# Performance work log

Hardware: AMD Instinct MI355X
Metric: run time of the kernel (lower is better)

The kernel has to match this reference:

```python
import jax, jax.numpy as jnp
import numpy as np
import math

E = 2048         # n_embd
H = 16           # num query head pairs (num_heads)
HKV = 8          # num_kv_heads
NREP = H // HKV  # 2
HD = E // H // 2 # head_dim = 64
DEPTH = 12
LAMBDA_INIT = 0.8 - 0.6 * math.exp(-0.3 * DEPTH)
EPS = 1e-6


def setup_inputs() -> dict:
    key = jax.random.key(0)
    ks = jax.random.split(key, 10)
    s = lambda fan_in: 1.0 / np.sqrt(fan_in)
    return {
        "x": jax.random.normal(ks[0], (2, 2048, E), jnp.float32),
        "Wq": jax.random.normal(ks[1], (E, E), jnp.float32) * s(E),
        "Wk": jax.random.normal(ks[2], (E, E // NREP), jnp.float32) * s(E),
        "Wv": jax.random.normal(ks[3], (E, E // NREP), jnp.float32) * s(E),
        "Wo": jax.random.normal(ks[4], (E, E), jnp.float32) * s(E),
        "lam_q1": jax.random.normal(ks[5], (HD,), jnp.float32) * 0.1,
        "lam_k1": jax.random.normal(ks[6], (HD,), jnp.float32) * 0.1,
        "lam_q2": jax.random.normal(ks[7], (HD,), jnp.float32) * 0.1,
        "lam_k2": jax.random.normal(ks[8], (HD,), jnp.float32) * 0.1,
        "g": jnp.ones((2 * HD,), jnp.float32),  # RMSNorm weight
    }


def _rotary(x, cos, sin):
    # x: [B, T, nh, HD]; cos/sin: [T, HD//2]
    d = x.shape[-1] // 2
    x1, x2 = x[..., :d], x[..., d:]
    c = cos[None, :, None, :]
    si = sin[None, :, None, :]
    return jnp.concatenate([x1 * c + x2 * si, -x1 * si + x2 * c], axis=-1)


def reference(x, Wq, Wk, Wv, Wo, lam_q1, lam_k1, lam_q2, lam_k2, g):
    B, T, _ = x.shape
    q = (x @ Wq).reshape(B, T, 2 * H, HD)
    k = (x @ Wk).reshape(B, T, 2 * HKV, HD)
    v = (x @ Wv).reshape(B, T, HKV, 2 * HD)

    inv_freq = 1.0 / (10000.0 ** (jnp.arange(0, HD, 2, dtype=jnp.float32) / HD))
    freqs = jnp.arange(T, dtype=jnp.float32)[:, None] * inv_freq[None, :]
    cos, sin = jnp.cos(freqs), jnp.sin(freqs)
    q = _rotary(q, cos, sin)
    k = _rotary(k, cos, sin)

    q = jnp.transpose(q, (0, 2, 1, 3)) * (HD ** -0.5)   # [B, 2H, T, HD]
    k = jnp.repeat(jnp.transpose(k, (0, 2, 1, 3)), NREP, axis=1)  # [B, 2H, T, HD]
    v = jnp.repeat(jnp.transpose(v, (0, 2, 1, 3)), NREP, axis=1)  # [B, H, T, 2HD]

    scores = jnp.einsum('bhtd,bhsd->bhts', q, k)
    scores = jnp.nan_to_num(scores)
    mask = jnp.triu(jnp.full((T, T), -jnp.inf, scores.dtype), 1)
    scores = scores + mask
    p = jax.nn.softmax(scores.astype(jnp.float32), axis=-1).astype(scores.dtype)

    lam1 = jnp.exp(jnp.sum(lam_q1 * lam_k1))
    lam2 = jnp.exp(jnp.sum(lam_q2 * lam_k2))
    lam = lam1 - lam2 + LAMBDA_INIT

    p = p.reshape(B, H, 2, T, T)
    diff = p[:, :, 0] - lam * p[:, :, 1]               # [B, H, T, T]
    attn = jnp.einsum('bhts,bhsd->bhtd', diff, v)      # [B, H, T, 2HD]

    # RMSNorm over last dim (2*HD)
    attn = attn * jax.lax.rsqrt(jnp.mean(attn * attn, axis=-1, keepdims=True) + EPS) * g
    attn = attn * (1.0 - LAMBDA_INIT)
    attn = jnp.transpose(attn, (0, 2, 1, 3)).reshape(B, T, E)
    return attn @ Wo
```

## Files before the change

### kernel.cpp

```cpp
#include <hip/hip_runtime.h>

#define T_SEQ 2048

typedef __bf16 bf16x8 __attribute__((ext_vector_type(8)));
typedef float f32x4 __attribute__((ext_vector_type(4)));
typedef unsigned short u16;

__device__ __forceinline__ u16 f2b(float f) {
  unsigned u = __float_as_uint(f);
  unsigned r = 0x7fffu + ((u >> 16) & 1u);
  return (u16)((u + r) >> 16);
}
__device__ __forceinline__ float b2f(u16 v) {
  return __uint_as_float(((unsigned)v) << 16);
}
__device__ __forceinline__ f32x4 mfma16(bf16x8 a, bf16x8 b, f32x4 c) {
  return __builtin_amdgcn_mfma_f32_16x16x32_bf16(a, b, c, 0, 0, 0);
}
__device__ __forceinline__ unsigned pkhi(float lo, float hi) {
  return __builtin_amdgcn_perm(__float_as_uint(hi), __float_as_uint(lo), 0x07060302u);
}
#if defined(__has_builtin)
#if __has_builtin(__builtin_amdgcn_exp2f)
#define HAVE_RAW_EXP2 1
#endif
#endif
__device__ __forceinline__ float exp2r(float x) {
#ifdef HAVE_RAW_EXP2
  return __builtin_amdgcn_exp2f(x);
#else
  float r;
  asm("v_exp_f32 %0, %1" : "=v"(r) : "v"(x));
  return r;
#endif
}
__device__ __forceinline__ void glds16(const void* g, void* s) {
  __builtin_amdgcn_global_load_lds(
      (const __attribute__((address_space(1))) void*)(uintptr_t)g,
      (__attribute__((address_space(3))) void*)(unsigned)(uintptr_t)s, 16, 0, 0);
}

__global__ void lam_kernel(const float* __restrict__ q1, const float* __restrict__ k1,
                           const float* __restrict__ q2, const float* __restrict__ k2,
                           float* __restrict__ outp) {
  int l = threadIdx.x;
  float a = q1[l] * k1[l];
  float c = q2[l] * k2[l];
  #pragma unroll
  for (int off = 32; off > 0; off >>= 1) {
    a += __shfl_down(a, off);
    c += __shfl_down(c, off);
  }
  if (l == 0) outp[0] = expf(a) - expf(c) + 0.7836057665316244f;
}

__global__ __launch_bounds__(256) void convert_kernel(const float* __restrict__ in,
                                                      u16* __restrict__ outp, int n) {
  int i = (blockIdx.x * 256 + threadIdx.x) * 4;
  if (i >= n) return;
  float4 v = *(const float4*)(in + i);
  ushort4 pk;
  pk.x = f2b(v.x); pk.y = f2b(v.y); pk.z = f2b(v.z); pk.w = f2b(v.w);
  *(ushort4*)(outp + i) = pk;
}

__global__ __launch_bounds__(256) void transposeW_kernel(const float* __restrict__ Wq,
                                                         const float* __restrict__ Wk,
                                                         const float* __restrict__ Wv,
                                                         const float* __restrict__ Wo,
                                                         u16* __restrict__ outp) {
  __shared__ float tile[32][33];
  const int ro0 = blockIdx.y * 32;
  const int r0 = blockIdx.x * 32;
  const float* src; int C, cbase;
  if (ro0 < 2048)      { src = Wq; C = 2048; cbase = 0; }
  else if (ro0 < 3072) { src = Wk; C = 1024; cbase = 2048; }
  else if (ro0 < 4096) { src = Wv; C = 1024; cbase = 3072; }
  else                 { src = Wo; C = 2048; cbase = 4096; }
  const int cs0 = ro0 - cbase;
  const int tx = threadIdx.x & 31, ty = threadIdx.x >> 5;
  #pragma unroll
  for (int k2 = 0; k2 < 4; k2++)
    tile[ty * 4 + k2][tx] = src[(size_t)(r0 + ty * 4 + k2) * C + cs0 + tx];
  __syncthreads();
  #pragma unroll
  for (int k2 = 0; k2 < 4; k2++)
    outp[(size_t)(ro0 + ty * 4 + k2) * 2048 + r0 + tx] = f2b(tile[tx][ty * 4 + k2]);
}

template <bool OUT_BF16>
__global__ __launch_bounds__(256) void gemm128_kernel(const u16* __restrict__ A,
                                                      const u16* __restrict__ BT,
                                                      void* __restrict__ C, int N, int K) {
  __shared__ alignas(16) u16 As[128 * 64];
  __shared__ alignas(16) u16 Bs[128 * 64];
  const int tid = threadIdx.x, w = tid >> 6, lane = tid & 63;
  const int l15 = lane & 15, quad = lane >> 4;
  const int m0 = blockIdx.y * 128, n0 = blockIdx.x * 128;
  const int wm = (w >> 1) * 64, wn = (w & 1) * 64;
  const int lr = lane >> 3, slot = lane & 7, csw = slot ^ lr;
  f32x4 acc[4][4];
  #pragma unroll
  for (int mt = 0; mt < 4; mt++)
    #pragma unroll
    for (int nt = 0; nt < 4; nt++) acc[mt][nt] = (f32x4){0.f, 0.f, 0.f, 0.f};
  const u16* Ag = A + (size_t)(m0 + w * 32 + lr) * K + csw * 8;
  const u16* Bg = BT + (size_t)(n0 + w * 32 + lr) * K + csw * 8;
  u16* Asd = As + (w * 32) * 64;
  u16* Bsd = Bs + (w * 32) * 64;
  for (int kt = 0; kt < K; kt += 64) {
    #pragma unroll
    for (int i = 0; i < 4; i++) {
      glds16(Ag + kt + (size_t)(i * 8) * K, Asd + i * 512);
      glds16(Bg + kt + (size_t)(i * 8) * K, Bsd + i * 512);
    }
    __syncthreads();
    #pragma unroll
    for (int kk = 0; kk < 2; kk++) {
      bf16x8 am[4], bn[4];
      #pragma unroll
      for (int t = 0; t < 4; t++) {
        const int ra = wm + t * 16 + l15;
        am[t] = *(const bf16x8*)&As[ra * 64 + (((kk * 4 + quad) ^ (ra & 7)) << 3)];
        const int rb = wn + t * 16 + l15;
        bn[t] = *(const bf16x8*)&Bs[rb * 64 + (((kk * 4 + quad) ^ (rb & 7)) << 3)];
      }
      #pragma unroll
      for (int mt = 0; mt < 4; mt++)
        #pragma unroll
        for (int nt = 0; nt < 4; nt++) acc[mt][nt] = mfma16(am[mt], bn[nt], acc[mt][nt]);
    }
    __syncthreads();
  }
  const int row = m0 + wm + quad * 4;
  #pragma unroll
  for (int mt = 0; mt < 4; mt++) {
    #pragma unroll
    for (int nt = 0; nt < 4; nt++) {
      const int col = n0 + wn + nt * 16 + l15;
      #pragma unroll
      for (int rr = 0; rr < 4; rr++) {
        if (OUT_BF16)
          ((u16*)C)[(size_t)(row + mt * 16 + rr) * N + col] = f2b(acc[mt][nt][rr]);
        else
          ((float*)C)[(size_t)(row + mt * 16 + rr) * N + col] = acc[mt][nt][rr];
      }
    }
  }
}

__global__ __launch_bounds__(256) void rotary_kernel(const u16* __restrict__ qkv,
                                                     u16* __restrict__ Qb,
                                                     u16* __restrict__ Kb, float qscale) {
  int idx = blockIdx.x * 256 + threadIdx.x;
  int i = idx & 31;
  int bt = (idx >> 5) & 4095;
  int hh = idx >> 17;
  int t = bt & (T_SEQ - 1), b = bt >> 11;
  bool isq = hh < 32;
  int col = isq ? hh * 64 : 2048 + (hh - 32) * 64;
  size_t inb = (size_t)bt * 4096 + col + i;
  float x1 = b2f(qkv[inb]);
  float x2 = b2f(qkv[inb + 32]);
  float invf = exp2f(-(float)i * 0.4152410118609203f);
  float ang = (float)t * invf;
  float c = cosf(ang), s = sinf(ang);
  float scale = isq ? qscale : 1.0f;
  float o1 = (x1 * c + x2 * s) * scale;
  float o2 = (x2 * c - x1 * s) * scale;
  u16* outp = isq ? (Qb + (size_t)(b * 32 + hh) * (T_SEQ * 64))
                  : (Kb + (size_t)(b * 16 + hh - 32) * (T_SEQ * 64));
  size_t ob = (size_t)t * 64 + i;
  outp[ob] = f2b(o1);
  outp[ob + 32] = f2b(o2);
}

__global__ __launch_bounds__(256) void vtrans_kernel(const u16* __restrict__ qkv,
                                                     u16* __restrict__ outp) {
  __shared__ unsigned tile[32][33];
  int bh = blockIdx.z;
  int t0 = blockIdx.x * 32, dv0 = blockIdx.y * 32;
  int tx = threadIdx.x & 31, ty = threadIdx.x >> 5;
  int bt_base = (bh >> 3) * T_SEQ;
  int col = 3072 + (bh & 7) * 128 + dv0 + tx;
  #pragma unroll
  for (int k2 = 0; k2 < 4; k2++)
    tile[ty * 4 + k2][tx] = qkv[(size_t)(bt_base + t0 + ty * 4 + k2) * 4096 + col];
  __syncthreads();
  const int stile = t0 >> 6, sin = (t0 & 63) + tx;
  #pragma unroll
  for (int k2 = 0; k2 < 4; k2++) {
    int dv = dv0 + ty * 4 + k2;
    outp[(((size_t)bh * 32 + stile) * 128 + dv) * 64 + sin] = (u16)tile[tx][ty * 4 + k2];
  }
}

__global__ __launch_bounds__(256) void attn_kernel(const u16* __restrict__ Qb,
                                                   const u16* __restrict__ Kb,
                                                   const u16* __restrict__ Vt,
                                                   const float* __restrict__ lamp,
                                                   const float* __restrict__ g,
                                                   u16* __restrict__ attn_out) {
  __shared__ alignas(16) u16 Ks[64 * 64];
  __shared__ alignas(16) u16 Vs[128 * 64];
  __shared__ alignas(16) u16 Ps[4][16][136];
  const int pr = blockIdx.x;
  const int bh = blockIdx.y;
  const int b = bh >> 4, h = bh & 15;
  const int tid = threadIdx.x, w = tid >> 6, lane = tid & 63;
  const int l15 = lane & 15, quad = lane >> 4;
  const int lr = lane >> 3, slot = lane & 7, csw = slot ^ lr;
  const float lam = lamp[0];

  const u16* Kg = Kb + (size_t)(b * 16 + h) * (T_SEQ * 64) + (w * 16 + lr) * 64 + csw * 8;
  const u16* Vg = Vt + (size_t)(b * 8 + (h >> 1)) * (T_SEQ * 128) + w * 2048 + lr * 64 + csw * 8;
  u16* kd = &Ks[w * 1024];
  u16* vd = &Vs[w * 2048];

  #pragma unroll 1
  for (int half = 0; half < 2; half++) {
    const int tt = half ? 31 - pr : pr;
    const int qb = tt * 64 + w * 16;
    const int qglob = qb + l15;

    bf16x8 qf[2][2];
    #pragma unroll
    for (int e = 0; e < 2; e++)
      #pragma unroll
      for (int kk = 0; kk < 2; kk++)
        qf[e][kk] = *(const bf16x8*)&Qb[((size_t)(b * 32 + 2 * h + e) * T_SEQ + qb + l15) * 64 +
                                        kk * 32 + quad * 8];

    f32x4 o[2][8];
    float lsum[2] = {0.f, 0.f};
    #pragma unroll
    for (int e = 0; e < 2; e++)
      #pragma unroll
      for (int nt = 0; nt < 8; nt++) o[e][nt] = (f32x4){0.f, 0.f, 0.f, 0.f};

    for (int st = 0; st <= tt; st++) {
      const u16* kp = Kg + st * 4096;
      const u16* vp = Vg + st * 8192;
      glds16(kp, kd); glds16(kp + 512, kd + 512);
      glds16(vp, vd); glds16(vp + 512, vd + 512);
      glds16(vp + 1024, vd + 1024); glds16(vp + 1536, vd + 1536);
      __syncthreads();

      bf16x8 kf[4][2];
      #pragma unroll
      for (int j = 0; j < 4; j++) {
        const int rk = j * 16 + l15;
        #pragma unroll
        for (int kk = 0; kk < 2; kk++)
          kf[j][kk] = *(const bf16x8*)&Ks[rk * 64 + (((kk * 4 + quad) ^ (rk & 7)) << 3)];
      }

      #pragma unroll
      for (int e = 0; e < 2; e++) {
        f32x4 sc[4];
        #pragma unroll
        for (int j = 0; j < 4; j++) {
          f32x4 z = {0.f, 0.f, 0.f, 0.f};
          z = mfma16(kf[j][0], qf[e][0], z);
          sc[j] = mfma16(kf[j][1], qf[e][1], z);
        }
        if (st == tt) {
          #pragma unroll
          for (int j = 0; j < 4; j++) {
            int srow = st * 64 + j * 16 + quad * 4;
            #pragma unroll
            for (int rr = 0; rr < 4; rr++)
              if (srow + rr > qglob) sc[j][rr] = -1e30f;
          }
        }
        float ls = 0.f;
        #pragma unroll
        for (int j = 0; j < 4; j++) {
          #pragma unroll
          for (int rr = 0; rr < 4; rr++) {
            float p = exp2r(sc[j][rr]);
            sc[j][rr] = p;
            ls += p;
          }
          uint2 pk;
          pk.x = pkhi(sc[j][0], sc[j][1]);
          pk.y = pkhi(sc[j][2], sc[j][3]);
          *(uint2*)&Ps[w][l15][e * 64 + j * 16 + quad * 4] = pk;
        }
        lsum[e] += ls;
      }
      asm volatile("s_waitcnt lgkmcnt(0)" ::: "memory");
      bf16x8 pa[2][2];
      #pragma unroll
      for (int e = 0; e < 2; e++)
        #pragma unroll
        for (int kk = 0; kk < 2; kk++)
          pa[e][kk] = *(const bf16x8*)&Ps[w][l15][e * 64 + kk * 32 + quad * 8];
      asm volatile("" ::: "memory");
      #pragma unroll
      for (int nt = 0; nt < 8; nt++) {
        const int rv = nt * 16 + l15;
        bf16x8 vf0 = *(const bf16x8*)&Vs[rv * 64 + ((quad ^ (rv & 7)) << 3)];
        bf16x8 vf1 = *(const bf16x8*)&Vs[rv * 64 + (((4 + quad) ^ (rv & 7)) << 3)];
        o[0][nt] = mfma16(vf0, pa[0][0], o[0][nt]);
        o[0][nt] = mfma16(vf1, pa[0][1], o[0][nt]);
        o[1][nt] = mfma16(vf0, pa[1][0], o[1][nt]);
        o[1][nt] = mfma16(vf1, pa[1][1], o[1][nt]);
      }
      __syncthreads();
    }

    float l0 = lsum[0], l1 = lsum[1];
    l0 += __shfl_xor(l0, 16); l0 += __shfl_xor(l0, 32);
    l1 += __shfl_xor(l1, 16); l1 += __shfl_xor(l1, 32);
    const float il0 = 1.f / l0, il1 = lam / l1;
    float ssq = 0.f;
    #pragma unroll
    for (int nt = 0; nt < 8; nt++)
      #pragma unroll
      for (int rr = 0; rr < 4; rr++) {
        float v = o[0][nt][rr] * il0 - o[1][nt][rr] * il1;
        o[0][nt][rr] = v;
        ssq += v * v;
      }
    ssq += __shfl_xor(ssq, 16);
    ssq += __shfl_xor(ssq, 32);
    const float rsc = rsqrtf(ssq * (1.f / 128.f) + 1e-6f) * 0.2163942334683756f;
    #pragma unroll
    for (int nt = 0; nt < 8; nt++) {
      float4 gv = *(const float4*)&g[nt * 16 + quad * 4];
      uint2 pk;
      pk.x = (unsigned)f2b(o[0][nt][0] * rsc * gv.x) |
             ((unsigned)f2b(o[0][nt][1] * rsc * gv.y) << 16);
      pk.y = (unsigned)f2b(o[0][nt][2] * rsc * gv.z) |
             ((unsigned)f2b(o[0][nt][3] * rsc * gv.w) << 16);
      *(uint2*)&Ps[w][l15][nt * 16 + quad * 4] = pk;
    }
    asm volatile("s_waitcnt lgkmcnt(0)" ::: "memory");
    #pragma unroll
    for (int i = 0; i < 4; i++) {
      const int r = (lane >> 4) + i * 4, c = (lane & 15) * 8;
      bf16x8 ov = *(const bf16x8*)&Ps[w][r][c];
      *(bf16x8*)&attn_out[(size_t)(b * T_SEQ + qb + r) * 2048 + h * 128 + c] = ov;
    }
    __syncthreads();
  }
}

extern "C" void kernel_launch(void* const* d_in, const int* in_sizes, int n_in, void* d_out,
                              int out_size, void* d_ws, size_t ws_size, hipStream_t stream) {
  const float* x = (const float*)d_in[0];
  const float* Wq = (const float*)d_in[1];
  const float* Wk = (const float*)d_in[2];
  const float* Wv = (const float*)d_in[3];
  const float* Wo = (const float*)d_in[4];
  const float* lq1 = (const float*)d_in[5];
  const float* lk1 = (const float*)d_in[6];
  const float* lq2 = (const float*)d_in[7];
  const float* lk2 = (const float*)d_in[8];
  const float* g = (const float*)d_in[9];

  char* ws = (char*)d_ws;
  u16* WT = (u16*)(ws);
  u16* xbf = (u16*)(ws + 25165824);
  u16* QKV = (u16*)(ws + 41943040);
  u16* Qb = (u16*)(ws + 75497472);
  u16* Kb = (u16*)(ws + 92274688);
  u16* Vt = (u16*)(ws + 100663296);
  u16* Attn = (u16*)(ws + 109051904);
  float* lam = (float*)(ws + 125829120);

  lam_kernel<<<1, 64, 0, stream>>>(lq1, lk1, lq2, lk2, lam);
  convert_kernel<<<8192, 256, 0, stream>>>(x, xbf, 8388608);
  transposeW_kernel<<<dim3(64, 192), 256, 0, stream>>>(Wq, Wk, Wv, Wo, WT);
  gemm128_kernel<true><<<dim3(32, 32), 256, 0, stream>>>(xbf, WT, QKV, 4096, 2048);
  rotary_kernel<<<24576, 256, 0, stream>>>(QKV, Qb, Kb, 0.18033688011112042f);
  vtrans_kernel<<<dim3(64, 4, 16), 256, 0, stream>>>(QKV, Vt);
  attn_kernel<<<dim3(16, 32), 256, 0, stream>>>(Qb, Kb, Vt, lam, g, Attn);
  gemm128_kernel<false><<<dim3(16, 32), 256, 0, stream>>>(Attn, WT + (size_t)4096 * 2048, d_out,
                                                          2048, 2048);
}
```

Baseline: 365.7 us.

## Add 256x256 tiled QKV GEMM with phased LDS pipelining and priority scheduling

Replaces the 128x128 QKV projection GEMM with a new 512-thread kernel that computes 256x256 output tiles. It stages half-tiles into double-buffered LDS directly from global memory and interleaves those loads with MFMA phases, using barriers, setprio and explicit waitcnt. The goal is more data reuse per block and better overlap of global loads with matrix math. The cost is 128KB of LDS per block and a 16x16 grid of 256 blocks, which may leave some CUs idle, plus fragile hand-written synchronization.

New measurement: 337.8 us. 1.08x faster.

```diff
diff --git a/kernel.cpp b/kernel.cpp
--- a/kernel.cpp
+++ b/kernel.cpp
@@ -147,6 +147,102 @@
       }
     }
   }
+}
+
+#define STAGE_HALF(TILE, ROLE, BUF)                                                     \
+  do {                                                                                  \
+    const u16* sp_ = ((ROLE) == 0 || (ROLE) == 3 ? Ag : Bg) +                           \
+                     (size_t)((ROLE) >= 2 ? 128 : 0) * K + (size_t)(TILE) * 64;         \
+    u16* dp_ = ((ROLE) == 0 || (ROLE) == 3 ? &As[BUF][0] : &Bs[BUF][0]) +               \
+               (((ROLE) >= 2 ? 128 : 0) + w * 8) * 64;                                  \
+    glds16(sp_, dp_);                                                                   \
+    glds16(sp_ + (size_t)64 * K, dp_ + 4096);                                           \
+  } while (0)
+
+#define PHASE(I, J, BUF, NEWA, NEWB, BN, STILE, SROLE, SBUF, DOVM)                      \
+  do {                                                                                  \
+    if (NEWA) {                                                                         \
+      _Pragma("unroll") for (int u_ = 0; u_ < 4; u_++) {                                \
+        const int ar_ = ((I) * 4 + u_) * 32 + wm * 16 + l15;                            \
+        _Pragma("unroll") for (int kk_ = 0; kk_ < 2; kk_++)                             \
+            am[u_][kk_] = *(const bf16x8*)&As[BUF][ar_ * 64 +                           \
+                              (((kk_ * 4 + quad) ^ (ar_ & 7)) << 3)];                   \
+      }                                                                                 \
+    }                                                                                   \
+    if (NEWB) {                                                                         \
+      _Pragma("unroll") for (int v_ = 0; v_ < 2; v_++) {                                \
+        const int br_ = ((J) * 2 + v_) * 64 + wn * 16 + l15;                            \
+        _Pragma("unroll") for (int kk_ = 0; kk_ < 2; kk_++)                             \
+            BN[v_][kk_] = *(const bf16x8*)&Bs[BUF][br_ * 64 +                           \
+                              (((kk_ * 4 + quad) ^ (br_ & 7)) << 3)];                   \
+      }                                                                                 \
+    }                                                                                   \
+    STAGE_HALF(STILE, SROLE, SBUF);                                                     \
+    __builtin_amdgcn_s_barrier();                                                       \
+    asm volatile("s_waitcnt lgkmcnt(0)" ::: "memory");                                  \
+    __builtin_amdgcn_sched_barrier(0);                                                  \
+    __builtin_amdgcn_s_setprio(1);                                                      \
+    _Pragma("unroll") for (int u_ = 0; u_ < 4; u_++)                                    \
+        _Pragma("unroll") for (int v_ = 0; v_ < 2; v_++) {                              \
+      acc[(I) * 4 + u_][(J) * 2 + v_] =                                                 \
+          mfma16(am[u_][0], BN[v_][0], acc[(I) * 4 + u_][(J) * 2 + v_]);                \
+      acc[(I) * 4 + u_][(J) * 2 + v_] =                                                 \
+          mfma16(am[u_][1], BN[v_][1], acc[(I) * 4 + u_][(J) * 2 + v_]);                \
+    }                                                                                   \
+    __builtin_amdgcn_s_setprio(0);                                                      \
+    if (DOVM) asm volatile("s_waitcnt vmcnt(6)" ::: "memory");                          \
+    __builtin_amdgcn_s_barrier();                                                       \
+  } while (0)
+
+__global__ __launch_bounds__(512, 2) void gemm256_kernel(const u16* __restrict__ A,
+                                                         const u16* __restrict__ BT,
+                                                         u16* __restrict__ C, int N, int K) {
+  __shared__ alignas(16) u16 As[2][256 * 64];
+  __shared__ alignas(16) u16 Bs[2][256 * 64];
+  const int tid = threadIdx.x, w = tid >> 6, lane = tid & 63;
+  const int l15 = lane & 15, quad = lane >> 4;
+  const int wm = w >> 2, wn = w & 3;
+  const int lr = lane >> 3, slot = lane & 7, csw = slot ^ lr;
+  const int m0 = blockIdx.y * 256, n0 = blockIdx.x * 256;
+  const int nkt = K >> 6;
+
+  f32x4 acc[8][4];
+  #pragma unroll
+  for (int r = 0; r < 8; r++)
+    #pragma unroll
+    for (int s = 0; s < 4; s++) acc[r][s] = (f32x4){0.f, 0.f, 0.f, 0.f};
+
+  const u16* Ag = A + (size_t)(m0 + w * 8 + lr) * K + csw * 8;
+  const u16* Bg = BT + (size_t)(n0 + w * 8 + lr) * K + csw * 8;
+
+  bf16x8 am[4][2], bn0[2][2], bn1[2][2];
+
+  STAGE_HALF(0, 0, 0); STAGE_HALF(0, 1, 0); STAGE_HALF(0, 2, 0); STAGE_HALF(0, 3, 0);
+  STAGE_HALF(1, 0, 1); STAGE_HALF(1, 1, 1); STAGE_HALF(1, 2, 1);
+  asm volatile("s_waitcnt vmcnt(6)" ::: "memory");
+  __builtin_amdgcn_s_barrier();
+
+  #pragma unroll 1
+  for (int t = 0; t < nkt; t += 2) {
+    PHASE(0, 0, 0, 1, 1, bn0, t + 1, 3, 1, 0);
+    PHASE(0, 1, 0, 0, 1, bn1, t + 2, 0, 0, 0);
+    PHASE(1, 0, 0, 1, 0, bn0, t + 2, 1, 0, 0);
+    PHASE(1, 1, 0, 0, 0, bn1, t + 2, 2, 0, 1);
+    PHASE(0, 0, 1, 1, 1, bn0, t + 2, 3, 0, 0);
+    PHASE(0, 1, 1, 0, 1, bn1, t + 3, 0, 1, 0);
+    PHASE(1, 0, 1, 1, 0, bn0, t + 3, 1, 1, 0);
+    PHASE(1, 1, 1, 0, 0, bn1, t + 3, 2, 1, 1);
+  }
+
+  const int crow = m0 + wm * 16 + quad * 4;
+  const int ccol = n0 + wn * 16 + l15;
+  #pragma unroll
+  for (int r = 0; r < 8; r++)
+    #pragma unroll
+    for (int s = 0; s < 4; s++)
+      #pragma unroll
+      for (int rr = 0; rr < 4; rr++)
+        C[(size_t)(crow + r * 32 + rr) * N + ccol + s * 64] = f2b(acc[r][s][rr]);
 }
 
 __global__ __launch_bounds__(256) void rotary_kernel(const u16* __restrict__ qkv,
@@ -373,7 +469,7 @@
   lam_kernel<<<1, 64, 0, stream>>>(lq1, lk1, lq2, lk2, lam);
   convert_kernel<<<8192, 256, 0, stream>>>(x, xbf, 8388608);
   transposeW_kernel<<<dim3(64, 192), 256, 0, stream>>>(Wq, Wk, Wv, Wo, WT);
-  gemm128_kernel<true><<<dim3(32, 32), 256, 0, stream>>>(xbf, WT, QKV, 4096, 2048);
+  gemm256_kernel<<<dim3(16, 16), 512, 0, stream>>>(xbf, WT, QKV, 4096, 2048);
   rotary_kernel<<<24576, 256, 0, stream>>>(QKV, Qb, Kb, 0.18033688011112042f);
   vtrans_kernel<<<dim3(64, 4, 16), 256, 0, stream>>>(QKV, Vt);
   attn_kernel<<<dim3(16, 32), 256, 0, stream>>>(Qb, Kb, Vt, lam, g, Attn);
```
